# Kernel optimization log

Measured on AMD Instinct MI355X. Metric: run time of the kernel, lower is better.

## Reference

```python
import jax, jax.numpy as jnp
import numpy as np

N, E, F, H, C, G, NC = 50000, 800000, 128, 3, 64, 16, 10
NEG_SLOPE = 0.2


def gatv2_layer(x, src, dst, Wl, Wr, att, b, concat):
    # PyG GATv2Conv (share_weights=False, add_self_loops already in src/dst)
    n = x.shape[0]
    h, c = att.shape
    xl = (x @ Wl).reshape(n, h, c)   # source-side transform
    xr = (x @ Wr).reshape(n, h, c)   # target-side transform
    # per-edge attention logits: a^T LeakyReLU(xl_j + xr_i)
    e = jax.nn.leaky_relu(xl[src] + xr[dst], NEG_SLOPE)          # [E,h,c]
    logits = jnp.einsum('ehc,hc->eh', e, att)                    # [E,h]
    # segment softmax over incoming edges of each target node
    m = jax.ops.segment_max(logits, dst, num_segments=n)
    m = jnp.where(jnp.isfinite(m), m, jnp.zeros_like(m))
    p = jnp.exp(logits - m[dst])
    denom = jax.ops.segment_sum(p, dst, num_segments=n)
    alpha = p / jnp.maximum(denom[dst], 1e-16)                   # [E,h]
    out = jax.ops.segment_sum(alpha[:, :, None] * xl[src], dst, num_segments=n)
    out = out.reshape(n, h * c) if concat else out.mean(axis=1)
    return out + b


def setup_inputs() -> dict:
    key = jax.random.key(0)
    ks = jax.random.split(key, 16)
    glorot = lambda k, shp: jax.random.normal(k, shp, jnp.float32) * np.sqrt(2.0 / (shp[0] + shp[-1]))
    return {
        'x': jax.random.normal(ks[0], (N, F), jnp.float32),
        'edge_index': jax.random.randint(ks[1], (2, E), 0, N, jnp.int64),
        'batch': jnp.sort(jax.random.randint(ks[2], (N,), 0, G, jnp.int64)),
        'Wl1': glorot(ks[3], (F, H * C)),
        'Wr1': glorot(ks[4], (F, H * C)),
        'att1': glorot(ks[5], (H, C)),
        'b1': jnp.zeros((H * C,), jnp.float32),
        'Wl2': glorot(ks[6], (H * C, H * C)),
        'Wr2': glorot(ks[7], (H * C, H * C)),
        'att2': glorot(ks[8], (H, C)),
        'b2': jnp.zeros((C,), jnp.float32),
        'Wc': glorot(ks[9], (C, NC)),
        'bc': jnp.zeros((NC,), jnp.float32),
    }


def reference(x, edge_index, batch, Wl1, Wr1, att1, b1, Wl2, Wr2, att2, b2, Wc, bc):
    n = x.shape[0]
    loops = jnp.arange(n, dtype=edge_index.dtype)
    src = jnp.concatenate([edge_index[0], loops])  # add self loops (PyG default)
    dst = jnp.concatenate([edge_index[1], loops])
    h = jax.nn.relu(gatv2_layer(x, src, dst, Wl1, Wr1, att1, b1, True))
    # dropout is identity in eval mode
    h = jax.nn.relu(gatv2_layer(h, src, dst, Wl2, Wr2, att2, b2, False))
    # global mean pool over graph ids
    sums = jax.ops.segment_sum(h, batch, num_segments=G)
    counts = jax.ops.segment_sum(jnp.ones((n, 1), h.dtype), batch, num_segments=G)
    pooled = sums / jnp.maximum(counts, 1.0)
    logits = pooled @ Wc + bc
    return jax.nn.softmax(logits, axis=1)
```

## Files before the change

kernel.cpp:

```cpp
#include <hip/hip_runtime.h>
#include <hip/hip_bf16.h>
#include <stdint.h>

#define NN 50000
#define EE 800000
#define FF 128
#define HH 3
#define CC 64
#define GG 16
#define NCLS 10
#define HC (HH*CC)

#define LOG2E 1.4426950408889634f

typedef uint16_t u16;
typedef __attribute__((ext_vector_type(8))) short short8;
typedef __attribute__((ext_vector_type(4))) float f32x4;

__device__ __forceinline__ u16 bf16_rne(float x) {
    uint32_t u = __float_as_uint(x);
    u += 0x7fffu + ((u >> 16) & 1u);
    return (u16)(u >> 16);
}
__device__ __forceinline__ void split2(float x, u16& h, u16& l) {
    h = bf16_rne(x);
    float fh = __uint_as_float((uint32_t)h << 16);
    l = bf16_rne(x - fh);
}

__device__ __forceinline__ float qsum16(float x) {
    #define DPP_ADD(ctrl) \
        x += __int_as_float(__builtin_amdgcn_update_dpp(0, __float_as_int(x), ctrl, 0xf, 0xf, true))
    DPP_ADD(0x111);
    DPP_ADD(0x112);
    DPP_ADD(0x114);
    DPP_ADD(0x118);
    #undef DPP_ADD
    return __int_as_float(__builtin_amdgcn_ds_swizzle(__float_as_int(x), 0x1F0));
}

__device__ __forceinline__ void unpack12(uint4 q0, uint2 q1, float v[3][4]) {
    v[0][0] = __uint_as_float(q0.x << 16);
    v[1][0] = __uint_as_float(q0.x & 0xffff0000u);
    v[2][0] = __uint_as_float(q0.y << 16);
    v[0][1] = __uint_as_float(q0.y & 0xffff0000u);
    v[1][1] = __uint_as_float(q0.z << 16);
    v[2][1] = __uint_as_float(q0.z & 0xffff0000u);
    v[0][2] = __uint_as_float(q0.w << 16);
    v[1][2] = __uint_as_float(q0.w & 0xffff0000u);
    v[2][2] = __uint_as_float(q1.x << 16);
    v[0][3] = __uint_as_float(q1.x & 0xffff0000u);
    v[1][3] = __uint_as_float(q1.y << 16);
    v[2][3] = __uint_as_float(q1.y & 0xffff0000u);
}

__global__ void count_deg(const int* __restrict__ dst, int* __restrict__ deg, int E) {
    int i = blockIdx.x * blockDim.x + threadIdx.x;
    if (i < E) atomicAdd(&deg[dst[i]], 1);
}

__global__ __launch_bounds__(256) void scan_local(const int* __restrict__ deg,
                                                  int* __restrict__ rowp1,
                                                  int* __restrict__ partials, int n) {
    __shared__ int sums[256];
    int base = blockIdx.x * 2048 + threadIdx.x * 8;
    int v[8]; int run = 0;
    #pragma unroll
    for (int i = 0; i < 8; ++i) {
        int x = (base + i < n) ? deg[base + i] + 1 : 0;
        run += x; v[i] = run;
    }
    sums[threadIdx.x] = run;
    __syncthreads();
    for (int off = 1; off < 256; off <<= 1) {
        int t = (threadIdx.x >= off) ? sums[threadIdx.x - off] : 0;
        __syncthreads();
        sums[threadIdx.x] += t;
        __syncthreads();
    }
    int prefix = (threadIdx.x > 0) ? sums[threadIdx.x - 1] : 0;
    #pragma unroll
    for (int i = 0; i < 8; ++i)
        if (base + i < n) rowp1[base + i] = v[i] + prefix;
    if (threadIdx.x == 255) partials[blockIdx.x] = sums[255];
}

__global__ void scan_partials(int* partials, int nb) {
    if (threadIdx.x == 0 && blockIdx.x == 0) {
        int run = 0;
        for (int b = 0; b < nb; ++b) { int t = partials[b]; partials[b] = run; run += t; }
    }
}

__global__ void scan_finish(int* __restrict__ rowp, int* __restrict__ cursor,
                            const int* __restrict__ partials, int n) {
    int i = blockIdx.x * blockDim.x + threadIdx.x;
    if (i == 0) { rowp[0] = 0; cursor[0] = 0; }
    if (i < n) {
        int v = rowp[1 + i] + partials[i / 2048];
        rowp[1 + i] = v;
        if (i < n - 1) cursor[i + 1] = v;
    }
}

__global__ void fill_csr(const int* __restrict__ src, const int* __restrict__ dst,
                         int* __restrict__ cursor, int* __restrict__ colv, int E) {
    int i = blockIdx.x * blockDim.x + threadIdx.x;
    if (i < E) {
        int pos = atomicAdd(&cursor[dst[i]], 1);
        colv[pos] = src[i];
    }
}

__global__ void add_self(const int* __restrict__ rowp, int* __restrict__ colv, int n) {
    int i = blockIdx.x * blockDim.x + threadIdx.x;
    if (i < n) colv[rowp[i + 1] - 1] = i;
}

__global__ void prep_all(const float* __restrict__ Wl1, const float* __restrict__ Wr1,
                         const float* __restrict__ Wl2, const float* __restrict__ Wr2,
                         u16* l1h, u16* l1l, u16* r1h, u16* r1l,
                         u16* l2h, u16* l2l, u16* r2h, u16* r2l) {
    int idx = blockIdx.x * blockDim.x + threadIdx.x;
    const int S1 = FF * HC, S2 = HC * HC;
    const float* B; u16 *H, *L; int K, f;
    if (idx < S1)                { B = Wl1; H = l1h; L = l1l; K = FF; f = idx; }
    else if (idx < 2*S1)         { B = Wr1; H = r1h; L = r1l; K = FF; f = idx - S1; }
    else if (idx < 2*S1 + S2)    { B = Wl2; H = l2h; L = l2l; K = HC; f = idx - 2*S1; }
    else if (idx < 2*S1 + 2*S2)  { B = Wr2; H = r2h; L = r2l; K = HC; f = idx - 2*S1 - S2; }
    else return;
    const int KB = K / 32;
    int j    = f & 7;
    int lane = (f >> 3) & 63;
    int rest = f >> 9;
    int kb    = rest % KB;
    int ntile = rest / KB;
    int n = ntile * 16 + (lane & 15);
    int k = kb * 32 + (lane >> 4) * 8 + j;
    u16 h, l; split2(B[k * HC + n], h, l);
    H[f] = h;
    L[f] = l;
}

template<int K, bool SPLITIN>
__global__ __launch_bounds__(256) void mfma_gemm(
    const float* __restrict__ Af,
    const u16* __restrict__ Ahi, const u16* __restrict__ Alo,
    const u16* __restrict__ B1h, const u16* __restrict__ B1l,
    const u16* __restrict__ B2h, const u16* __restrict__ B2l,
    u16* __restrict__ C1p, u16* __restrict__ C2p, int M)
{
    constexpr int KB = K / 32;
    __shared__ __align__(16) u16 smem[32 * 256];

    const int tid  = threadIdx.x;
    const int w    = tid >> 6;
    const int lane = tid & 63;
    const int m0   = blockIdx.x * 32;
    const int frow = lane & 15;
    const int fkc  = lane >> 4;

    f32x4 acc[2][3][2];
    #pragma unroll
    for (int mt = 0; mt < 2; ++mt)
        #pragma unroll
        for (int nt = 0; nt < 3; ++nt)
            #pragma unroll
            for (int rt = 0; rt < 2; ++rt)
                acc[mt][nt][rt] = (f32x4){0.f, 0.f, 0.f, 0.f};

    int arow[2];
    arow[0] = min(m0 + frow, M - 1);
    arow[1] = min(m0 + 16 + frow, M - 1);

    const u16* bb[2][3][2];
    #pragma unroll
    for (int mt = 0; mt < 2; ++mt) {
        const u16* Bh = mt ? B2h : B1h;
        const u16* Bl = mt ? B2l : B1l;
        #pragma unroll
        for (int nt = 0; nt < 3; ++nt) {
            size_t o = ((size_t)(w * 3 + nt) * KB * 64 + lane) * 8;
            bb[mt][nt][0] = Bh + o;
            bb[mt][nt][1] = Bl + o;
        }
    }

    #pragma unroll
    for (int kb = 0; kb < KB; ++kb) {
        short8 afh[2], afl[2];
        #pragma unroll
        for (int rt = 0; rt < 2; ++rt) {
            if constexpr (SPLITIN) {
                const float* ap = Af + (size_t)arow[rt] * K + kb * 32 + fkc * 8;
                float4 a0 = *(const float4*)ap;
                float4 a1 = *(const float4*)(ap + 4);
                ushort4 h0, l0, h1, l1;
                split2(a0.x, h0.x, l0.x); split2(a0.y, h0.y, l0.y);
                split2(a0.z, h0.z, l0.z); split2(a0.w, h0.w, l0.w);
                split2(a1.x, h1.x, l1.x); split2(a1.y, h1.y, l1.y);
                split2(a1.z, h1.z, l1.z); split2(a1.w, h1.w, l1.w);
                afh[rt] = (short8){(short)h0.x, (short)h0.y, (short)h0.z, (short)h0.w,
                                   (short)h1.x, (short)h1.y, (short)h1.z, (short)h1.w};
                afl[rt] = (short8){(short)l0.x, (short)l0.y, (short)l0.z, (short)l0.w,
                                   (short)l1.x, (short)l1.y, (short)l1.z, (short)l1.w};
            } else {
                size_t o = (size_t)arow[rt] * K + kb * 32 + fkc * 8;
                afh[rt] = *(const short8*)(Ahi + o);
                afl[rt] = *(const short8*)(Alo + o);
            }
        }
        #pragma unroll
        for (int mt = 0; mt < 2; ++mt) {
            #pragma unroll
            for (int nt = 0; nt < 3; ++nt) {
                short8 bh = *(const short8*)(bb[mt][nt][0] + kb * 512);
                short8 bl = *(const short8*)(bb[mt][nt][1] + kb * 512);
                #pragma unroll
                for (int rt = 0; rt < 2; ++rt)
                    acc[mt][nt][rt] = __builtin_amdgcn_mfma_f32_16x16x32_bf16(afh[rt], bh, acc[mt][nt][rt], 0, 0, 0);
                #pragma unroll
                for (int rt = 0; rt < 2; ++rt)
                    acc[mt][nt][rt] = __builtin_amdgcn_mfma_f32_16x16x32_bf16(afh[rt], bl, acc[mt][nt][rt], 0, 0, 0);
                #pragma unroll
                for (int rt = 0; rt < 2; ++rt)
                    acc[mt][nt][rt] = __builtin_amdgcn_mfma_f32_16x16x32_bf16(afl[rt], bh, acc[mt][nt][rt], 0, 0, 0);
            }
        }
    }

    const int q4 = (lane >> 4) * 4;
    #pragma unroll
    for (int mt = 0; mt < 2; ++mt) {
        __syncthreads();
        #pragma unroll
        for (int nt = 0; nt < 3; ++nt) {
            int col = w * 48 + nt * 16 + frow;
            int c = col & 63, h = col >> 6;
            int u = c * 3 + h;
            int chunk = u >> 3, within = u & 7;
            #pragma unroll
            for (int rt = 0; rt < 2; ++rt)
                #pragma unroll
                for (int r = 0; r < 4; ++r) {
                    int lrow = rt * 16 + q4 + r;
                    smem[lrow * 256 + ((chunk ^ (lrow & 7)) << 3) + within] =
                        bf16_rne(acc[mt][nt][rt][r]);
                }
        }
        __syncthreads();
        u16* C = mt ? C2p : C1p;
        #pragma unroll
        for (int i = 0; i < 3; ++i) {
            int idx  = tid + 256 * i;
            int lrow = idx / 24;
            int coff = idx % 24;
            if (m0 + lrow < M)
                *(uint4*)(C + (size_t)(m0 + lrow) * HC + coff * 8) =
                    *(const uint4*)&smem[lrow * 256 + ((coff ^ (lrow & 7)) << 3)];
        }
    }
}

template<bool MASK>
__device__ __forceinline__ void gat_quad(
    int i0, int q, int l, int beg, int cnt, int cm1,
    const int* __restrict__ colv, const u16* __restrict__ xlp,
    const float attv[3][4], const float xrv[3][4],
    float s[3], float acc[3][4])
{
    int idx = i0 + q;
    int iq  = MASK ? min(idx, cm1) : idx;
    int src = colv[beg + iq];
    const u16* p = xlp + (size_t)src * HC + l * 12;
    uint4 q0 = *(const uint4*)p;
    uint2 q1 = *(const uint2*)(p + 8);
    float v[3][4];
    unpack12(q0, q1, v);
    #pragma unroll
    for (int r = 0; r < 3; ++r) {
        float t0 = v[r][0] + xrv[r][0]; t0 = fmaxf(t0, 0.2f * t0);
        float t1 = v[r][1] + xrv[r][1]; t1 = fmaxf(t1, 0.2f * t1);
        float t2 = v[r][2] + xrv[r][2]; t2 = fmaxf(t2, 0.2f * t2);
        float t3 = v[r][3] + xrv[r][3]; t3 = fmaxf(t3, 0.2f * t3);
        float d = t0 * attv[r][0];
        d = fmaf(t1, attv[r][1], d);
        d = fmaf(t2, attv[r][2], d);
        d = fmaf(t3, attv[r][3], d);
        d = qsum16(d);
        float pe = __builtin_amdgcn_exp2f(d);
        if (MASK) pe = (idx < cnt) ? pe : 0.f;
        s[r] += pe;
        acc[r][0] = fmaf(pe, v[r][0], acc[r][0]);
        acc[r][1] = fmaf(pe, v[r][1], acc[r][1]);
        acc[r][2] = fmaf(pe, v[r][2], acc[r][2]);
        acc[r][3] = fmaf(pe, v[r][3], acc[r][3]);
    }
}

template<int CONCAT>
__global__ __launch_bounds__(256) void gat_agg(
    const u16* __restrict__ xlp, const u16* __restrict__ xrp,
    const int* __restrict__ rowp, const int* __restrict__ colv,
    const float* __restrict__ att, const float* __restrict__ bias,
    float* __restrict__ out, u16* __restrict__ ohi, u16* __restrict__ olo, int n)
{
    const int wave = threadIdx.x >> 6;
    const int lane = threadIdx.x & 63;
    const int node = __builtin_amdgcn_readfirstlane(blockIdx.x * 4 + wave);
    if (node >= n) return;
    const int q = lane >> 4;
    const int l = lane & 15;

    float attv[3][4], xrv[3][4];
    #pragma unroll
    for (int r = 0; r < 3; ++r) {
        float4 a4 = *(const float4*)(att + r * 64 + 4 * l);
        attv[r][0] = a4.x * LOG2E; attv[r][1] = a4.y * LOG2E;
        attv[r][2] = a4.z * LOG2E; attv[r][3] = a4.w * LOG2E;
    }
    {
        const u16* p = xrp + (size_t)node * HC + l * 12;
        uint4 x0 = *(const uint4*)p;
        uint2 x1 = *(const uint2*)(p + 8);
        unpack12(x0, x1, xrv);
    }

    float s[3] = {0.f, 0.f, 0.f};
    float acc[3][4] = {{0.f}};

    const int beg = rowp[node];
    const int cnt = rowp[node + 1] - beg;
    const int cm1 = cnt - 1;

    int i0 = 0;
    const int nfull = cnt & ~3;
    #pragma unroll 2
    for (; i0 < nfull; i0 += 4)
        gat_quad<false>(i0, q, l, beg, cnt, cm1, colv, xlp, attv, xrv, s, acc);
    if (i0 < cnt)
        gat_quad<true>(i0, q, l, beg, cnt, cm1, colv, xlp, attv, xrv, s, acc);

    #pragma unroll
    for (int r = 0; r < 3; ++r) {
        s[r] += __shfl_xor(s[r], 16, 64);
        s[r] += __shfl_xor(s[r], 32, 64);
        #pragma unroll
        for (int j = 0; j < 4; ++j) {
            acc[r][j] += __shfl_xor(acc[r][j], 16, 64);
            acc[r][j] += __shfl_xor(acc[r][j], 32, 64);
        }
    }

    if (CONCAT) {
        if (lane < 48) {
            int r = lane >> 4, ll = lane & 15;
            float inv = 1.f / s[r];
            float4 bv = *(const float4*)(bias + r * 64 + 4 * ll);
            ushort4 hv, lv;
            float o0 = fmaxf(fmaf(acc[r][0], inv, bv.x), 0.f); split2(o0, hv.x, lv.x);
            float o1 = fmaxf(fmaf(acc[r][1], inv, bv.y), 0.f); split2(o1, hv.y, lv.y);
            float o2 = fmaxf(fmaf(acc[r][2], inv, bv.z), 0.f); split2(o2, hv.z, lv.z);
            float o3 = fmaxf(fmaf(acc[r][3], inv, bv.w), 0.f); split2(o3, hv.w, lv.w);
            size_t ob = (size_t)node * HC + r * 64 + 4 * ll;
            *(ushort4*)&ohi[ob] = hv;
            *(ushort4*)&olo[ob] = lv;
        }
    } else {
        if (lane < 16) {
            float i0v = 1.f / s[0], i1v = 1.f / s[1], i2v = 1.f / s[2];
            float4 bv = *(const float4*)(bias + 4 * l);
            float4 o;
            o.x = fmaxf((acc[0][0]*i0v + acc[1][0]*i1v + acc[2][0]*i2v) * (1.f/3.f) + bv.x, 0.f);
            o.y = fmaxf((acc[0][1]*i0v + acc[1][1]*i1v + acc[2][1]*i2v) * (1.f/3.f) + bv.y, 0.f);
            o.z = fmaxf((acc[0][2]*i0v + acc[1][2]*i1v + acc[2][2]*i2v) * (1.f/3.f) + bv.z, 0.f);
            o.w = fmaxf((acc[0][3]*i0v + acc[1][3]*i1v + acc[2][3]*i2v) * (1.f/3.f) + bv.w, 0.f);
            *(float4*)&out[(size_t)node * CC + 4 * l] = o;
        }
    }
}

#define POOL_BLOCKS 384
__global__ __launch_bounds__(256) void pool_kernel(
    const float* __restrict__ h2, const int* __restrict__ batch,
    float* __restrict__ pool, float* __restrict__ cnt, int n)
{
    const int c   = threadIdx.x & 63;
    const int sub = threadIdx.x >> 6;
    const int per = (n + gridDim.x - 1) / gridDim.x;
    const int n0  = blockIdx.x * per;
    const int n1  = min(n0 + per, n);

    float run = 0.f;
    float crun = 0.f;
    int curg = -1;
    for (int node = n0 + sub; node < n1; node += 4) {
        int g = batch[node];
        if (g != curg) {
            if (curg >= 0) {
                atomicAdd(&pool[curg * CC + c], run);
                if (c == 0) atomicAdd(&cnt[curg], crun);
            }
            run = 0.f; crun = 0.f; curg = g;
        }
        run += h2[(size_t)node * CC + c];
        crun += 1.f;
    }
    if (curg >= 0) {
        atomicAdd(&pool[curg * CC + c], run);
        if (c == 0) atomicAdd(&cnt[curg], crun);
    }
}

__global__ void head_kernel(const float* __restrict__ pool, const float* __restrict__ cnt,
                            const float* __restrict__ Wc, const float* __restrict__ bc,
                            float* __restrict__ outp) {
    __shared__ float lg[GG][NCLS];
    int t = threadIdx.x;
    if (t < GG * NCLS) {
        int g = t / NCLS, k = t % NCLS;
        float invc = 1.f / fmaxf(cnt[g], 1.f);
        float a = 0.f;
        for (int c = 0; c < CC; ++c) a += pool[g * CC + c] * Wc[c * NCLS + k];
        lg[g][k] = a * invc + bc[k];
    }
    __syncthreads();
    if (t < GG) {
        float mx = -1e30f;
        for (int k = 0; k < NCLS; ++k) mx = fmaxf(mx, lg[t][k]);
        float ssum = 0.f; float e[NCLS];
        for (int k = 0; k < NCLS; ++k) { e[k] = __expf(lg[t][k] - mx); ssum += e[k]; }
        for (int k = 0; k < NCLS; ++k) outp[t * NCLS + k] = e[k] / ssum;
    }
}

extern "C" void kernel_launch(void* const* d_in, const int* in_sizes, int n_in,
                              void* d_out, int out_size, void* d_ws, size_t ws_size,
                              hipStream_t stream) {
    const float* x     = (const float*)d_in[0];
    const int*   ei    = (const int*)d_in[1];
    const int*   batch = (const int*)d_in[2];
    const float* Wl1   = (const float*)d_in[3];
    const float* Wr1   = (const float*)d_in[4];
    const float* att1  = (const float*)d_in[5];
    const float* b1    = (const float*)d_in[6];
    const float* Wl2   = (const float*)d_in[7];
    const float* Wr2   = (const float*)d_in[8];
    const float* att2  = (const float*)d_in[9];
    const float* b2    = (const float*)d_in[10];
    const float* Wc    = (const float*)d_in[11];
    const float* bc    = (const float*)d_in[12];

    const int n = in_sizes[2];
    const int E = in_sizes[1] / 2;
    const int* srcv = ei;
    const int* dstv = ei + E;

    char* base = (char*)d_ws;
    size_t off = 0;
    auto alloc = [&](size_t bytes) -> char* {
        char* p = base + off;
        off = (off + bytes + 255) & ~(size_t)255;
        return p;
    };
    int*   deg      = (int*)  alloc((size_t)n * 4);
    int*   cursor   = (int*)  alloc((size_t)n * 4);
    int*   rowp     = (int*)  alloc((size_t)(n + 1) * 4);
    int*   partials = (int*)  alloc(256 * 4);
    int*   colv     = (int*)  alloc((size_t)(E + n) * 4);
    u16*   xlp      = (u16*)  alloc((size_t)n * HC * 2);
    u16*   xrp      = (u16*)  alloc((size_t)n * HC * 2);
    u16*   bufHi    = (u16*)  alloc((size_t)n * HC * 2);
    u16*   bufLo    = (u16*)  alloc((size_t)n * HC * 2);
    float* h2       = (float*)alloc((size_t)n * CC * 4);
    float* pool     = (float*)alloc((size_t)GG * (CC + 1) * 4);
    float* cnt      = pool + GG * CC;
    u16*   Bl1hi    = (u16*)  alloc((size_t)FF * HC * 2);
    u16*   Bl1lo    = (u16*)  alloc((size_t)FF * HC * 2);
    u16*   Br1hi    = (u16*)  alloc((size_t)FF * HC * 2);
    u16*   Br1lo    = (u16*)  alloc((size_t)FF * HC * 2);
    u16*   Bl2hi    = (u16*)  alloc((size_t)HC * HC * 2);
    u16*   Bl2lo    = (u16*)  alloc((size_t)HC * HC * 2);
    u16*   Br2hi    = (u16*)  alloc((size_t)HC * HC * 2);
    u16*   Br2lo    = (u16*)  alloc((size_t)HC * HC * 2);

    hipMemsetAsync(deg, 0, (size_t)n * 4, stream);
    count_deg<<<(E + 255) / 256, 256, 0, stream>>>(dstv, deg, E);
    int nchunks = (n + 2047) / 2048;
    scan_local<<<nchunks, 256, 0, stream>>>(deg, rowp + 1, partials, n);
    scan_partials<<<1, 64, 0, stream>>>(partials, nchunks);
    scan_finish<<<(n + 255) / 256, 256, 0, stream>>>(rowp, cursor, partials, n);
    fill_csr<<<(E + 255) / 256, 256, 0, stream>>>(srcv, dstv, cursor, colv, E);
    add_self<<<(n + 255) / 256, 256, 0, stream>>>(rowp, colv, n);

    const int prep_total = 2 * FF * HC + 2 * HC * HC;
    prep_all<<<(prep_total + 255) / 256, 256, 0, stream>>>(
        Wl1, Wr1, Wl2, Wr2, Bl1hi, Bl1lo, Br1hi, Br1lo, Bl2hi, Bl2lo, Br2hi, Br2lo);

    const int gblocks = (n + 31) / 32;

    mfma_gemm<FF, true><<<gblocks, 256, 0, stream>>>(
        x, nullptr, nullptr, Bl1hi, Bl1lo, Br1hi, Br1lo, xlp, xrp, n);
    gat_agg<1><<<(n + 3) / 4, 256, 0, stream>>>(xlp, xrp, rowp, colv, att1, b1,
                                                nullptr, bufHi, bufLo, n);

    mfma_gemm<HC, false><<<gblocks, 256, 0, stream>>>(
        nullptr, bufHi, bufLo, Bl2hi, Bl2lo, Br2hi, Br2lo, xlp, xrp, n);
    gat_agg<0><<<(n + 3) / 4, 256, 0, stream>>>(xlp, xrp, rowp, colv, att2, b2,
                                                h2, nullptr, nullptr, n);

    hipMemsetAsync(pool, 0, (size_t)GG * (CC + 1) * 4, stream);
    pool_kernel<<<POOL_BLOCKS, 256, 0, stream>>>(h2, batch, pool, cnt, n);
    head_kernel<<<1, 256, 0, stream>>>(pool, cnt, Wc, bc, (float*)d_out);
}
```

Baseline: 352.9 us.

## Drop split-bf16 emulation in GEMMs and fuse small CSR/pool setup kernels

```diff
diff --git a/kernel.cpp b/kernel.cpp
--- a/kernel.cpp
+++ b/kernel.cpp
@@ -21,11 +21,6 @@
     uint32_t u = __float_as_uint(x);
     u += 0x7fffu + ((u >> 16) & 1u);
     return (u16)(u >> 16);
-}
-__device__ __forceinline__ void split2(float x, u16& h, u16& l) {
-    h = bf16_rne(x);
-    float fh = __uint_as_float((uint32_t)h << 16);
-    l = bf16_rne(x - fh);
 }
 
 __device__ __forceinline__ float qsum16(float x) {
@@ -85,20 +80,23 @@
     if (threadIdx.x == 255) partials[blockIdx.x] = sums[255];
 }
 
-__global__ void scan_partials(int* partials, int nb) {
-    if (threadIdx.x == 0 && blockIdx.x == 0) {
-        int run = 0;
-        for (int b = 0; b < nb; ++b) { int t = partials[b]; partials[b] = run; run += t; }
-    }
-}
-
-__global__ void scan_finish(int* __restrict__ rowp, int* __restrict__ cursor,
-                            const int* __restrict__ partials, int n) {
-    int i = blockIdx.x * blockDim.x + threadIdx.x;
+__global__ __launch_bounds__(256) void scan_finish(
+    int* __restrict__ rowp, int* __restrict__ cursor, const int* __restrict__ partials,
+    int* __restrict__ colv, int n, int nchunks) {
+    __shared__ int pre[32];
+    int t = threadIdx.x;
+    if (t < 32) {
+        int s = 0;
+        for (int b = 0; b < nchunks && b < t; ++b) s += partials[b];
+        pre[t] = s;
+    }
+    __syncthreads();
+    int i = blockIdx.x * blockDim.x + t;
     if (i == 0) { rowp[0] = 0; cursor[0] = 0; }
     if (i < n) {
-        int v = rowp[1 + i] + partials[i / 2048];
+        int v = rowp[1 + i] + pre[i >> 11];
         rowp[1 + i] = v;
+        colv[v - 1] = i;
         if (i < n - 1) cursor[i + 1] = v;
     }
 }
@@ -112,22 +110,18 @@
     }
 }
 
-__global__ void add_self(const int* __restrict__ rowp, int* __restrict__ colv, int n) {
-    int i = blockIdx.x * blockDim.x + threadIdx.x;
-    if (i < n) colv[rowp[i + 1] - 1] = i;
-}
-
 __global__ void prep_all(const float* __restrict__ Wl1, const float* __restrict__ Wr1,
                          const float* __restrict__ Wl2, const float* __restrict__ Wr2,
-                         u16* l1h, u16* l1l, u16* r1h, u16* r1l,
-                         u16* l2h, u16* l2l, u16* r2h, u16* r2l) {
+                         u16* l1, u16* r1, u16* l2, u16* r2,
+                         float* __restrict__ pool) {
     int idx = blockIdx.x * blockDim.x + threadIdx.x;
+    if (idx < GG * (CC + 1)) pool[idx] = 0.f;
     const int S1 = FF * HC, S2 = HC * HC;
-    const float* B; u16 *H, *L; int K, f;
-    if (idx < S1)                { B = Wl1; H = l1h; L = l1l; K = FF; f = idx; }
-    else if (idx < 2*S1)         { B = Wr1; H = r1h; L = r1l; K = FF; f = idx - S1; }
-    else if (idx < 2*S1 + S2)    { B = Wl2; H = l2h; L = l2l; K = HC; f = idx - 2*S1; }
-    else if (idx < 2*S1 + 2*S2)  { B = Wr2; H = r2h; L = r2l; K = HC; f = idx - 2*S1 - S2; }
+    const float* B; u16* H; int K, f;
+    if (idx < S1)                { B = Wl1; H = l1; K = FF; f = idx; }
+    else if (idx < 2*S1)         { B = Wr1; H = r1; K = FF; f = idx - S1; }
+    else if (idx < 2*S1 + S2)    { B = Wl2; H = l2; K = HC; f = idx - 2*S1; }
+    else if (idx < 2*S1 + 2*S2)  { B = Wr2; H = r2; K = HC; f = idx - 2*S1 - S2; }
     else return;
     const int KB = K / 32;
     int j    = f & 7;
@@ -137,17 +131,13 @@
     int ntile = rest / KB;
     int n = ntile * 16 + (lane & 15);
     int k = kb * 32 + (lane >> 4) * 8 + j;
-    u16 h, l; split2(B[k * HC + n], h, l);
-    H[f] = h;
-    L[f] = l;
-}
-
-template<int K, bool SPLITIN>
+    H[f] = bf16_rne(B[k * HC + n]);
+}
+
+template<int K, bool CVTIN>
 __global__ __launch_bounds__(256) void mfma_gemm(
-    const float* __restrict__ Af,
-    const u16* __restrict__ Ahi, const u16* __restrict__ Alo,
-    const u16* __restrict__ B1h, const u16* __restrict__ B1l,
-    const u16* __restrict__ B2h, const u16* __restrict__ B2l,
+    const float* __restrict__ Af, const u16* __restrict__ Ab,
+    const u16* __restrict__ B1, const u16* __restrict__ B2,
     u16* __restrict__ C1p, u16* __restrict__ C2p, int M)
 {
     constexpr int KB = K / 32;
@@ -173,60 +163,39 @@
     arow[0] = min(m0 + frow, M - 1);
     arow[1] = min(m0 + 16 + frow, M - 1);
 
-    const u16* bb[2][3][2];
-    #pragma unroll
-    for (int mt = 0; mt < 2; ++mt) {
-        const u16* Bh = mt ? B2h : B1h;
-        const u16* Bl = mt ? B2l : B1l;
-        #pragma unroll
-        for (int nt = 0; nt < 3; ++nt) {
-            size_t o = ((size_t)(w * 3 + nt) * KB * 64 + lane) * 8;
-            bb[mt][nt][0] = Bh + o;
-            bb[mt][nt][1] = Bl + o;
-        }
-    }
+    const u16* bb[2][3];
+    #pragma unroll
+    for (int mt = 0; mt < 2; ++mt)
+        #pragma unroll
+        for (int nt = 0; nt < 3; ++nt)
+            bb[mt][nt] = (mt ? B2 : B1) + ((size_t)(w * 3 + nt) * KB * 64 + lane) * 8;
 
     #pragma unroll
     for (int kb = 0; kb < KB; ++kb) {
-        short8 afh[2], afl[2];
+        short8 af[2];
         #pragma unroll
         for (int rt = 0; rt < 2; ++rt) {
-            if constexpr (SPLITIN) {
+            if constexpr (CVTIN) {
                 const float* ap = Af + (size_t)arow[rt] * K + kb * 32 + fkc * 8;
                 float4 a0 = *(const float4*)ap;
                 float4 a1 = *(const float4*)(ap + 4);
-                ushort4 h0, l0, h1, l1;
-                split2(a0.x, h0.x, l0.x); split2(a0.y, h0.y, l0.y);
-                split2(a0.z, h0.z, l0.z); split2(a0.w, h0.w, l0.w);
-                split2(a1.x, h1.x, l1.x); split2(a1.y, h1.y, l1.y);
-                split2(a1.z, h1.z, l1.z); split2(a1.w, h1.w, l1.w);
-                afh[rt] = (short8){(short)h0.x, (short)h0.y, (short)h0.z, (short)h0.w,
-                                   (short)h1.x, (short)h1.y, (short)h1.z, (short)h1.w};
-                afl[rt] = (short8){(short)l0.x, (short)l0.y, (short)l0.z, (short)l0.w,
-                                   (short)l1.x, (short)l1.y, (short)l1.z, (short)l1.w};
+                af[rt] = (short8){(short)bf16_rne(a0.x), (short)bf16_rne(a0.y),
+                                  (short)bf16_rne(a0.z), (short)bf16_rne(a0.w),
+                                  (short)bf16_rne(a1.x), (short)bf16_rne(a1.y),
+                                  (short)bf16_rne(a1.z), (short)bf16_rne(a1.w)};
             } else {
-                size_t o = (size_t)arow[rt] * K + kb * 32 + fkc * 8;
-                afh[rt] = *(const short8*)(Ahi + o);
-                afl[rt] = *(const short8*)(Alo + o);
+                af[rt] = *(const short8*)(Ab + (size_t)arow[rt] * K + kb * 32 + fkc * 8);
             }
         }
         #pragma unroll
-        for (int mt = 0; mt < 2; ++mt) {
+        for (int mt = 0; mt < 2; ++mt)
             #pragma unroll
             for (int nt = 0; nt < 3; ++nt) {
-                short8 bh = *(const short8*)(bb[mt][nt][0] + kb * 512);
-                short8 bl = *(const short8*)(bb[mt][nt][1] + kb * 512);
+                short8 b = *(const short8*)(bb[mt][nt] + kb * 512);
                 #pragma unroll
                 for (int rt = 0; rt < 2; ++rt)
-                    acc[mt][nt][rt] = __builtin_amdgcn_mfma_f32_16x16x32_bf16(afh[rt], bh, acc[mt][nt][rt], 0, 0, 0);
-                #pragma unroll
-                for (int rt = 0; rt < 2; ++rt)
-                    acc[mt][nt][rt] = __builtin_amdgcn_mfma_f32_16x16x32_bf16(afh[rt], bl, acc[mt][nt][rt], 0, 0, 0);
-                #pragma unroll
-                for (int rt = 0; rt < 2; ++rt)
-                    acc[mt][nt][rt] = __builtin_amdgcn_mfma_f32_16x16x32_bf16(afl[rt], bh, acc[mt][nt][rt], 0, 0, 0);
+                    acc[mt][nt][rt] = __builtin_amdgcn_mfma_f32_16x16x32_bf16(af[rt], b, acc[mt][nt][rt], 0, 0, 0);
             }
-        }
     }
 
     const int q4 = (lane >> 4) * 4;
@@ -303,7 +272,7 @@
     const u16* __restrict__ xlp, const u16* __restrict__ xrp,
     const int* __restrict__ rowp, const int* __restrict__ colv,
     const float* __restrict__ att, const float* __restrict__ bias,
-    float* __restrict__ out, u16* __restrict__ ohi, u16* __restrict__ olo, int n)
+    float* __restrict__ out, u16* __restrict__ oh1, int n)
 {
     const int wave = threadIdx.x >> 6;
     const int lane = threadIdx.x & 63;
@@ -357,14 +326,12 @@
             int r = lane >> 4, ll = lane & 15;
             float inv = 1.f / s[r];
             float4 bv = *(const float4*)(bias + r * 64 + 4 * ll);
-            ushort4 hv, lv;
-            float o0 = fmaxf(fmaf(acc[r][0], inv, bv.x), 0.f); split2(o0, hv.x, lv.x);
-            float o1 = fmaxf(fmaf(acc[r][1], inv, bv.y), 0.f); split2(o1, hv.y, lv.y);
-            float o2 = fmaxf(fmaf(acc[r][2], inv, bv.z), 0.f); split2(o2, hv.z, lv.z);
-            float o3 = fmaxf(fmaf(acc[r][3], inv, bv.w), 0.f); split2(o3, hv.w, lv.w);
-            size_t ob = (size_t)node * HC + r * 64 + 4 * ll;
-            *(ushort4*)&ohi[ob] = hv;
-            *(ushort4*)&olo[ob] = lv;
+            ushort4 hv;
+            hv.x = bf16_rne(fmaxf(fmaf(acc[r][0], inv, bv.x), 0.f));
+            hv.y = bf16_rne(fmaxf(fmaf(acc[r][1], inv, bv.y), 0.f));
+            hv.z = bf16_rne(fmaxf(fmaf(acc[r][2], inv, bv.z), 0.f));
+            hv.w = bf16_rne(fmaxf(fmaf(acc[r][3], inv, bv.w), 0.f));
+            *(ushort4*)&oh1[(size_t)node * HC + r * 64 + 4 * ll] = hv;
         }
     } else {
         if (lane < 16) {
@@ -470,46 +437,38 @@
     int*   colv     = (int*)  alloc((size_t)(E + n) * 4);
     u16*   xlp      = (u16*)  alloc((size_t)n * HC * 2);
     u16*   xrp      = (u16*)  alloc((size_t)n * HC * 2);
-    u16*   bufHi    = (u16*)  alloc((size_t)n * HC * 2);
-    u16*   bufLo    = (u16*)  alloc((size_t)n * HC * 2);
+    u16*   h1b      = (u16*)  alloc((size_t)n * HC * 2);
     float* h2       = (float*)alloc((size_t)n * CC * 4);
     float* pool     = (float*)alloc((size_t)GG * (CC + 1) * 4);
     float* cnt      = pool + GG * CC;
-    u16*   Bl1hi    = (u16*)  alloc((size_t)FF * HC * 2);
-    u16*   Bl1lo    = (u16*)  alloc((size_t)FF * HC * 2);
-    u16*   Br1hi    = (u16*)  alloc((size_t)FF * HC * 2);
-    u16*   Br1lo    = (u16*)  alloc((size_t)FF * HC * 2);
-    u16*   Bl2hi    = (u16*)  alloc((size_t)HC * HC * 2);
-    u16*   Bl2lo    = (u16*)  alloc((size_t)HC * HC * 2);
-    u16*   Br2hi    = (u16*)  alloc((size_t)HC * HC * 2);
-    u16*   Br2lo    = (u16*)  alloc((size_t)HC * HC * 2);
+    u16*   Bl1      = (u16*)  alloc((size_t)FF * HC * 2);
+    u16*   Br1      = (u16*)  alloc((size_t)FF * HC * 2);
+    u16*   Bl2      = (u16*)  alloc((size_t)HC * HC * 2);
+    u16*   Br2      = (u16*)  alloc((size_t)HC * HC * 2);
 
     hipMemsetAsync(deg, 0, (size_t)n * 4, stream);
     count_deg<<<(E + 255) / 256, 256, 0, stream>>>(dstv, deg, E);
     int nchunks = (n + 2047) / 2048;
     scan_local<<<nchunks, 256, 0, stream>>>(deg, rowp + 1, partials, n);
-    scan_partials<<<1, 64, 0, stream>>>(partials, nchunks);
-    scan_finish<<<(n + 255) / 256, 256, 0, stream>>>(rowp, cursor, partials, n);
+    scan_finish<<<(n + 255) / 256, 256, 0, stream>>>(rowp, cursor, partials, colv, n, nchunks);
     fill_csr<<<(E + 255) / 256, 256, 0, stream>>>(srcv, dstv, cursor, colv, E);
-    add_self<<<(n + 255) / 256, 256, 0, stream>>>(rowp, colv, n);
 
     const int prep_total = 2 * FF * HC + 2 * HC * HC;
     prep_all<<<(prep_total + 255) / 256, 256, 0, stream>>>(
-        Wl1, Wr1, Wl2, Wr2, Bl1hi, Bl1lo, Br1hi, Br1lo, Bl2hi, Bl2lo, Br2hi, Br2lo);
+        Wl1, Wr1, Wl2, Wr2, Bl1, Br1, Bl2, Br2, pool);
 
     const int gblocks = (n + 31) / 32;
 
     mfma_gemm<FF, true><<<gblocks, 256, 0, stream>>>(
-        x, nullptr, nullptr, Bl1hi, Bl1lo, Br1hi, Br1lo, xlp, xrp, n);
+        x, nullptr, Bl1, Br1, xlp, xrp, n);
     gat_agg<1><<<(n + 3) / 4, 256, 0, stream>>>(xlp, xrp, rowp, colv, att1, b1,
-                                                nullptr, bufHi, bufLo, n);
+                                                nullptr, h1b, n);
 
     mfma_gemm<HC, false><<<gblocks, 256, 0, stream>>>(
-        nullptr, bufHi, bufLo, Bl2hi, Bl2lo, Br2hi, Br2lo, xlp, xrp, n);
+        nullptr, h1b, Bl2, Br2, xlp, xrp, n);
     gat_agg<0><<<(n + 3) / 4, 256, 0, stream>>>(xlp, xrp, rowp, colv, att2, b2,
-                                                h2, nullptr, nullptr, n);
-
-    hipMemsetAsync(pool, 0, (size_t)GG * (CC + 1) * 4, stream);
+                                                h2, nullptr, n);
+
     pool_kernel<<<POOL_BLOCKS, 256, 0, stream>>>(h2, batch, pool, cnt, n);
     head_kernel<<<1, 256, 0, stream>>>(pool, cnt, Wc, bc, (float*)d_out);
 }
```

Result: faster. 332.7 us (-5.7%).
